# Performance work log

Measured on AMD Instinct MI355X. Metric: run time of the kernel, lower is better.

The kernel has to match this reference:

```python
import jax, jax.numpy as jnp
import numpy as np

B, Q, D_MODEL, H, D_HEAD, PAGE, N_PAGES = 8, 1024, 2048, 16, 128, 256, 8


def setup_inputs() -> dict:
    key = jax.random.key(0)
    ks = jax.random.split(key, 6)
    hidden_states = jax.random.normal(ks[0], (B, Q, D_MODEL), jnp.float32) * 0.02
    W_attn = jax.random.normal(ks[1], (D_MODEL, 3 * D_MODEL), jnp.float32) * 0.02
    b_attn = jnp.zeros((3 * D_MODEL,), jnp.float32)
    W_proj = jax.random.normal(ks[2], (D_MODEL, D_MODEL), jnp.float32) * 0.02
    b_proj = jnp.zeros((D_MODEL,), jnp.float32)
    k_pages = jax.random.normal(ks[3], (N_PAGES, B, H, PAGE, D_HEAD), jnp.float32)
    v_pages = jax.random.normal(ks[4], (N_PAGES, B, H, PAGE, D_HEAD), jnp.float32)
    # every cached page fully valid: (start=0, length=PAGE)
    page_pos = jnp.broadcast_to(jnp.array([0, PAGE], jnp.int32), (N_PAGES, B, 2))
    # current chunk: starts at end of cache, length = q_len
    input_pos = jnp.broadcast_to(jnp.array([N_PAGES * PAGE, Q], jnp.int32), (B, 2))
    return {
        "hidden_states": hidden_states,
        "W_attn": W_attn, "b_attn": b_attn,
        "W_proj": W_proj, "b_proj": b_proj,
        "k_pages": k_pages, "v_pages": v_pages,
        "page_pos": page_pos, "input_pos": input_pos,
    }


def reference(hidden_states, W_attn, b_attn, W_proj, b_proj,
              k_pages, v_pages, page_pos, input_pos):
    dtype = hidden_states.dtype
    NEG = jnp.finfo(dtype).min
    b, q_len, d_model = hidden_states.shape
    n_pages, _, num_heads, page_size, d_head = k_pages.shape
    scale = 1.0 / d_head ** 0.5

    # qkv projection (GPT2 c_attn)
    qkv = hidden_states @ W_attn + b_attn
    q, k_curr, v_curr = jnp.split(qkv, 3, axis=-1)

    def split_heads(x):  # [b, q, d_model] -> [b, h, q, d_head]
        return x.reshape(b, q_len, num_heads, d_head).transpose(0, 2, 1, 3)

    q = split_heads(q)
    k_curr = split_heads(k_curr)
    v_curr = split_heads(v_curr)

    # online softmax state
    m0 = jnp.full((b, num_heads, q_len, 1), NEG, dtype)
    l0 = jnp.zeros((b, num_heads, q_len, 1), dtype)
    acc0 = jnp.zeros((b, num_heads, q_len, d_head), dtype)

    kv_idx = jnp.arange(page_size)

    def page_step(carry, page):
        m, l, acc = carry
        k_p, v_p, pos = page  # [b,h,p,d], [b,h,p,d], [b,2]
        start, length = pos[:, 0], pos[:, 1]
        valid = (kv_idx[None, :] >= start[:, None]) & \
                (kv_idx[None, :] < (start + length)[:, None])  # [b, p]
        s = jnp.einsum('bhqd,bhpd->bhqp', q, k_p) * scale
        s = jnp.where(valid[:, None, None, :], s, NEG)
        m_p = s.max(axis=-1, keepdims=True)
        m_new = jnp.maximum(m, m_p)
        alpha = jnp.exp(m - m_new)
        e = jnp.exp(s - m_new)
        acc = alpha * acc + jnp.einsum('bhqp,bhpd->bhqd', e, v_p)
        l = alpha * l + e.sum(axis=-1, keepdims=True)
        return (m_new, l, acc), None

    (m, l, acc), _ = jax.lax.scan(page_step, (m0, l0, acc0),
                                  (k_pages, v_pages, page_pos))

    # final pass over current chunk: aligned start = 0, length from input_pos
    length = input_pos[:, 1]
    q_idx = jnp.arange(q_len)
    valid = q_idx[None, :] < length[:, None]                     # [b, q]
    causal = jnp.tril(jnp.ones((q_len, q_len), bool))            # keep lower tri
    s = jnp.einsum('bhqd,bhkd->bhqk', q, k_curr) * scale
    keep = valid[:, None, None, :] & causal[None, None, :, :]
    s = jnp.where(keep, s, NEG)
    m_p = s.max(axis=-1, keepdims=True)
    m_new = jnp.maximum(m, m_p)
    alpha = jnp.exp(m - m_new)
    e = jnp.exp(s - m_new)
    acc = alpha * acc + jnp.einsum('bhqk,bhkd->bhqd', e, v_curr)
    l = alpha * l + e.sum(axis=-1, keepdims=True)

    context = acc / jnp.maximum(l, 1e-9)
    context = context.transpose(0, 2, 1, 3).reshape(b, q_len, d_model)
    out = context @ W_proj + b_proj  # resid_dropout is identity in eval
    return out
```

## Files before the change

### kernel.cpp

```cpp
#include <hip/hip_runtime.h>

typedef __bf16 bf16;
typedef __bf16 bf16x8 __attribute__((ext_vector_type(8)));
typedef __bf16 bf16x4 __attribute__((ext_vector_type(4)));
typedef float f32x4 __attribute__((ext_vector_type(4)));
typedef unsigned short u16x4 __attribute__((ext_vector_type(4)));
typedef __attribute__((address_space(3))) const void as3_void;

#define GLOAD16(G,L) __builtin_amdgcn_global_load_lds((__attribute__((address_space(1))) const void*)(G), (__attribute__((address_space(3))) void*)(L), 16, 0, 0)

__global__ void k_cvt_bf16(const float* __restrict__ src, bf16* __restrict__ dst, int n4){
  int i = blockIdx.x*256 + threadIdx.x;
  if (i < n4){
    float4 v = reinterpret_cast<const float4*>(src)[i];
    bf16x4 o; o[0]=(bf16)v.x; o[1]=(bf16)v.y; o[2]=(bf16)v.z; o[3]=(bf16)v.w;
    reinterpret_cast<bf16x4*>(dst)[i] = o;
  }
}

__global__ void k_transpose_cvt(const float* __restrict__ src, bf16* __restrict__ dst, int K, int N){
  __shared__ float tile[32][33];
  int n0 = blockIdx.x*32, k0 = blockIdx.y*32;
  int tx = threadIdx.x & 31, ty = threadIdx.x >> 5;
  #pragma unroll
  for (int i=0;i<32;i+=8)
    tile[ty+i][tx] = src[(size_t)(k0+ty+i)*N + n0+tx];
  __syncthreads();
  #pragma unroll
  for (int i=0;i<32;i+=8)
    dst[(size_t)(n0+ty+i)*K + k0+tx] = (bf16)tile[tx][ty+i];
}

template<int EPI>
__global__ __launch_bounds__(256,2) void k_gemm(
    const bf16* __restrict__ A, const bf16* __restrict__ Bt,
    const float* __restrict__ bias, int N, int K,
    bf16* __restrict__ q_out, bf16* __restrict__ k_out, bf16* __restrict__ v_out,
    float* __restrict__ c_out)
{
  __shared__ bf16 As[2][128*32];
  __shared__ bf16 Bs[2][128*32];
  const int t = threadIdx.x, w = t>>6, l = t&63, g = l>>4;
  const int nb = N>>7;
  const int m0 = (blockIdx.x / nb)<<7, n0 = (blockIdx.x % nb)<<7;
  const bf16* Ab = A  + (size_t)m0*K;
  const bf16* Bb = Bt + (size_t)n0*K;
  size_t sOff[2];
  #pragma unroll
  for (int j=0;j<2;j++){
    int slot = t + (j<<8);
    sOff[j] = (size_t)(slot>>2)*K + ((slot&3)<<3);
  }
  auto stage = [&](int k0, int buf){
    char* ad = (char*)As + (buf<<13) + (w<<10);
    char* bd = (char*)Bs + (buf<<13) + (w<<10);
    #pragma unroll
    for (int j=0;j<2;j++){
      GLOAD16(Ab + sOff[j] + k0, ad + (j<<12));
      GLOAD16(Bb + sOff[j] + k0, bd + (j<<12));
    }
  };
  f32x4 acc[4][4] = {};
  const int mw = (w&1)<<6, nw = (w>>1)<<6;
  const int nk = K>>5;
  int buf = 0;
  stage(0, 0);
  asm volatile("s_waitcnt vmcnt(0)" ::: "memory");
  __syncthreads();
  for (int ks=0; ks<nk; ++ks){
    if (ks+1 < nk) stage((ks+1)<<5, buf^1);
    bf16x8 af[4], bfm[4];
    #pragma unroll
    for (int mf=0;mf<4;mf++)
      af[mf] = *reinterpret_cast<const bf16x8*>(&As[buf][(mw + mf*16 + (l&15))*32 + (g<<3)]);
    #pragma unroll
    for (int nf=0;nf<4;nf++)
      bfm[nf] = *reinterpret_cast<const bf16x8*>(&Bs[buf][(nw + nf*16 + (l&15))*32 + (g<<3)]);
    #pragma unroll
    for (int mf=0;mf<4;mf++)
      #pragma unroll
      for (int nf=0;nf<4;nf++)
        acc[mf][nf] = __builtin_amdgcn_mfma_f32_16x16x32_bf16(af[mf], bfm[nf], acc[mf][nf], 0,0,0);
    asm volatile("s_waitcnt vmcnt(0)" ::: "memory");
    __syncthreads();
    buf ^= 1;
  }
  if constexpr (EPI==0){
    #pragma unroll
    for (int nf=0;nf<4;nf++){
      const int col = n0 + nw + nf*16 + (l&15);
      const int sec = col>>11; const int rem = col&2047;
      const int hh = rem>>7;  const int dd = rem&127;
      bf16* dst = (sec==0) ? q_out : ((sec==1) ? k_out : v_out);
      const float bv = bias[col];
      #pragma unroll
      for (int mf=0;mf<4;mf++)
        #pragma unroll
        for (int ri=0;ri<4;ri++){
          const int row = m0 + mw + mf*16 + (g<<2) + ri;
          const int bb = row>>10, qp = row&1023;
          dst[(((size_t)(bb*16+hh)*1024 + qp)<<7) + dd] = (bf16)(acc[mf][nf][ri] + bv);
        }
    }
  } else {
    #pragma unroll
    for (int nf=0;nf<4;nf++){
      const int col = n0 + nw + nf*16 + (l&15);
      const float bv = bias[col];
      #pragma unroll
      for (int mf=0;mf<4;mf++)
        #pragma unroll
        for (int ri=0;ri<4;ri++){
          const int row = m0 + mw + mf*16 + (g<<2) + ri;
          c_out[(size_t)row*N + col] = acc[mf][nf][ri] + bv;
        }
    }
  }
}

__global__ __launch_bounds__(512) __attribute__((amdgpu_waves_per_eu(4,4))) void k_attn(
    const bf16* __restrict__ qb, const bf16* __restrict__ kb, const bf16* __restrict__ vb,
    const bf16* __restrict__ kpb, const bf16* __restrict__ vpb,
    const int* __restrict__ page_pos, const int* __restrict__ input_pos,
    bf16* __restrict__ ctx)
{
  __shared__ bf16 Ks[2*64*128];
  __shared__ bf16 Vs[2*64*128];
  const int t = threadIdx.x, w = t>>6, l = t&63, g = l>>4, c = l&15;
  const int bid = blockIdx.x;
  const int wg = (bid&7)*128 + (bid>>3);
  const int qt = wg & 7, h = (wg>>3)&15, b = wg>>7;
  const int q0w = (qt<<7) + (w<<4);
  const float scale2 = 0.12751743f;
  const size_t bh = (size_t)(b*16 + h);

  const bf16* qptr = qb + (bh<<17);
  bf16x8 qf[4];
  #pragma unroll
  for (int kc=0;kc<4;kc++)
    qf[kc] = *reinterpret_cast<const bf16x8*>(qptr + ((size_t)(q0w + c)<<7) + kc*32 + (g<<3));

  int kOff[2], vOff[2];
  #pragma unroll
  for (int j=0;j<2;j++){
    const int slot = t + (j<<9);
    {
      const int a = slot<<4; const int r = a>>8; const int co = (a&255) ^ ((r&7)<<4);
      kOff[j] = (r<<7) + (co>>1);
    }
    {
      const int s_ = slot;
      const int p  = ((s_>>6)<<2) | ((s_>>1)&3);
      const int d0 = (((s_>>3)&7)<<4) | ((s_&1)<<3);
      const int pp = (p&32) | ((p&4)<<2) | (((p>>3)&3)<<2) | (p&3);
      vOff[j] = (pp<<7) + d0;
    }
  }
  const bf16* kcb = kb + (bh<<17);
  const bf16* vcb = vb + (bh<<17);
  const int len_b = input_pos[b*2+1];
  const int NT = 32 + ((qt+1)<<1);

  f32x4 o[8] = {};
  float mrow = -1e38f;
  float lsum = 0.f;

  auto tsrc = [&](int T, const bf16*& ks, const bf16*& vs_){
    if (T < 32){
      size_t pb = ((((size_t)(T>>2)<<3) + (size_t)b)*16 + (size_t)h) << 15;
      size_t off = (size_t)(T&3)<<13;
      ks = kpb + pb + off; vs_ = vpb + pb + off;
    } else {
      int kt = T-32; ks = kcb + ((size_t)kt<<13); vs_ = vcb + ((size_t)kt<<13);
    }
  };
  auto stage = [&](int T, int buf){
    const bf16 *ks, *vs_; tsrc(T, ks, vs_);
    char* kd = (char*)Ks + (buf<<14) + (w<<10);
    char* vd = (char*)Vs + (buf<<14) + (w<<10);
    #pragma unroll
    for (int j=0;j<2;j++){
      GLOAD16(ks  + kOff[j], kd + (j<<13));
      GLOAD16(vs_ + vOff[j], vd + (j<<13));
    }
  };

  auto process = [&](int buf, int lo, int hi, bool masked, bool causal, int ktg){
    const char* Kb = (const char*)Ks + (buf<<14);
    const char* Vb = (const char*)Vs + (buf<<14);
    f32x4 s[4] = {};
    #pragma unroll
    for (int kc=0;kc<4;kc++){
      bf16x8 kf[4];
      #pragma unroll
      for (int cb=0;cb<4;cb++){
        const int krow = (cb<<4) + c;
        unsigned a = (unsigned)((krow<<8) + (kc<<6) + (g<<4)); a ^= (unsigned)((krow&7)<<4);
        kf[cb] = *reinterpret_cast<const bf16x8*>(Kb + a);
      }
      __builtin_amdgcn_s_setprio(1);
      #pragma unroll
      for (int cb=0;cb<4;cb++)
        s[cb] = __builtin_amdgcn_mfma_f32_16x16x32_bf16(kf[cb], qf[kc], s[cb], 0,0,0);
      __builtin_amdgcn_s_setprio(0);
    }
    if (masked){
      #pragma unroll
      for (int cb=0;cb<4;cb++)
        #pragma unroll
        for (int ri=0;ri<4;ri++){
          const int kvl = (cb<<4) + (g<<2) + ri;
          bool ok = (kvl >= lo) && (kvl < hi);
          if (causal) ok = ok && ((ktg + kvl) <= (q0w + c));
          s[cb][ri] = ok ? s[cb][ri]*scale2 : -3e38f;
        }
    } else {
      #pragma unroll
      for (int cb=0;cb<4;cb++)
        #pragma unroll
        for (int ri=0;ri<4;ri++)
          s[cb][ri] *= scale2;
    }
    {
      float mx = -3e38f;
      #pragma unroll
      for (int cb=0;cb<4;cb++)
        #pragma unroll
        for (int ri=0;ri<4;ri++) mx = fmaxf(mx, s[cb][ri]);
      mx = fmaxf(mx, __shfl_xor(mx, 16, 64));
      mx = fmaxf(mx, __shfl_xor(mx, 32, 64));
      const int defer = __all(mx - mrow <= 11.5f);
      if (!defer){
        const float mn = fmaxf(mrow, mx);
        const float al = exp2f(mrow - mn);
        mrow = mn;
        lsum *= al;
        #pragma unroll
        for (int ri=0;ri<4;ri++){
          const float av = __shfl(al, (l&48) | ((g<<2)+ri), 64);
          #pragma unroll
          for (int dcb=0;dcb<8;dcb++) o[dcb][ri] *= av;
        }
      }
      float ps = 0.f;
      #pragma unroll
      for (int cb=0;cb<4;cb++)
        #pragma unroll
        for (int ri=0;ri<4;ri++){
          const float e = exp2f(s[cb][ri] - mrow);
          s[cb][ri] = e; ps += e;
        }
      lsum += ps;
    }
    #pragma unroll
    for (int kc=0;kc<2;kc++){
      u16x4 vr0[8], vr1[8];
      #pragma unroll
      for (int dcb=0;dcb<8;dcb++){
        const unsigned sub = ((unsigned)((((kc<<3) + (g<<1))<<3) + dcb)<<7) + ((unsigned)c<<3);
        as3_void* pl = (as3_void*)(Vb + sub);
        asm volatile("ds_read_b64_tr_b16 %0, %2 offset:0\n\t"
                     "ds_read_b64_tr_b16 %1, %2 offset:1024"
                     : "=&v"(vr0[dcb]), "=&v"(vr1[dcb]) : "v"(pl) : "memory");
      }
      bf16x8 pav;
      #pragma unroll
      for (int e=0;e<8;e++)
        pav[e] = (bf16)s[(kc<<1)+(e>>2)][e&3];
      asm volatile("s_waitcnt lgkmcnt(0)" ::: "memory");
      __builtin_amdgcn_sched_barrier(0);
      __builtin_amdgcn_s_setprio(1);
      #pragma unroll
      for (int dcb=0;dcb<8;dcb++){
        union { unsigned short us[8]; bf16x8 v; } uu;
        #pragma unroll
        for (int i=0;i<4;i++){ uu.us[i]=vr0[dcb][i]; uu.us[4+i]=vr1[dcb][i]; }
        o[dcb] = __builtin_amdgcn_mfma_f32_16x16x32_bf16(pav, uu.v, o[dcb], 0,0,0);
      }
      __builtin_amdgcn_s_setprio(0);
    }
  };

  int buf = 0;
  stage(0, 0);
  asm volatile("s_waitcnt vmcnt(0)" ::: "memory");
  __syncthreads();
  for (int T=0; T<NT; ++T){
    if (T+1 < NT) stage(T+1, buf^1);
    int lo=0, hi=64, ktg=0; bool causal=false, masked=false, skip=false;
    if (T < 32){
      const int pg = T>>2, to = T&3;
      const int start = page_pos[(pg*8+b)*2], plen = page_pos[(pg*8+b)*2+1];
      lo = start - (to<<6); hi = start + plen - (to<<6); if (hi>64) hi=64;
      masked = (lo > 0) || (hi < 64);
      skip = (hi <= 0) || (lo >= 64);
    } else {
      const int kt = T-32; ktg = kt<<6;
      hi = len_b - ktg; if (hi>64) hi=64;
      skip = (ktg > q0w + 15) || (hi <= 0);
      causal = (ktg + 63 > q0w);
      masked = causal || (hi < 64);
    }
    if (!skip) process(buf, lo, hi, masked, causal, ktg);
    asm volatile("s_waitcnt vmcnt(0)" ::: "memory");
    __syncthreads();
    buf ^= 1;
  }

  {
    float tl = lsum;
    tl += __shfl_xor(tl, 16, 64);
    tl += __shfl_xor(tl, 32, 64);
    const float inv = 1.f / fmaxf(tl, 1e-9f);
    #pragma unroll
    for (int ri=0;ri<4;ri++){
      const float iv = __shfl(inv, (l&48) | ((g<<2)+ri), 64);
      const int q = q0w + (g<<2) + ri;
      #pragma unroll
      for (int dcb=0;dcb<8;dcb++)
        ctx[(((size_t)(b<<10) + q)<<11) + (h<<7) + (dcb<<4) + c] = (bf16)(o[dcb][ri]*iv);
    }
  }
}

extern "C" void kernel_launch(void* const* d_in, const int* in_sizes, int n_in,
                              void* d_out, int out_size, void* d_ws, size_t ws_size,
                              hipStream_t stream)
{
  const float* hidden  = (const float*)d_in[0];
  const float* W_attn  = (const float*)d_in[1];
  const float* b_attn  = (const float*)d_in[2];
  const float* W_proj  = (const float*)d_in[3];
  const float* b_proj  = (const float*)d_in[4];
  const float* k_pages = (const float*)d_in[5];
  const float* v_pages = (const float*)d_in[6];
  const int*   page_pos  = (const int*)d_in[7];
  const int*   input_pos = (const int*)d_in[8];
  float* out = (float*)d_out;
  char* ws = (char*)d_ws;
  bf16* A1  = (bf16*)(ws);
  bf16* Wt1 = (bf16*)(ws + 33554432);
  bf16* Wt2 = (bf16*)(ws + 58720256);
  bf16* qb  = (bf16*)(ws + 67108864);
  bf16* kb  = (bf16*)(ws + 100663296);
  bf16* vb  = (bf16*)(ws + 134217728);
  bf16* kpb = (bf16*)(ws + 167772160);
  bf16* vpb = (bf16*)(ws + 234881024);
  bf16* ctx = A1;

  k_cvt_bf16<<<16384, 256, 0, stream>>>(hidden, A1, 4194304);
  k_cvt_bf16<<<32768, 256, 0, stream>>>(k_pages, kpb, 8388608);
  k_cvt_bf16<<<32768, 256, 0, stream>>>(v_pages, vpb, 8388608);
  k_transpose_cvt<<<dim3(192,64), 256, 0, stream>>>(W_attn, Wt1, 2048, 6144);
  k_transpose_cvt<<<dim3(64,64),  256, 0, stream>>>(W_proj, Wt2, 2048, 2048);
  k_gemm<0><<<64*48, 256, 0, stream>>>(A1, Wt1, b_attn, 6144, 2048, qb, kb, vb, nullptr);
  k_attn<<<1024, 512, 0, stream>>>(qb, kb, vb, kpb, vpb, page_pos, input_pos, ctx);
  k_gemm<1><<<64*16, 256, 0, stream>>>(ctx, Wt2, b_proj, 2048, 2048, nullptr, nullptr, nullptr, out);
}
```

Before: 768.6 us.

## Rewrite GEMM with 256x256 tiles, 8 waves, swizzled LDS and interleaved staging

Replaces the 128x128, 4-wave GEMM with a 256x256 tile computed by 8 waves, using BK=64 and an XOR-swizzled LDS layout to avoid bank conflicts. The block index is remapped so neighbouring blocks share A and B rows, and each k-step is split into four MFMA clusters. Global-to-LDS prefetch of the next tile is spread between those clusters, with barriers and priority hints around the MFMA runs. This aims to raise arithmetic intensity and overlap loads with compute in both projection GEMMs. The cost is more registers per wave (8x4 accumulators) and fewer blocks (256 for the output projection), which may underfill the GPU.

```diff
diff --git a/kernel.cpp b/kernel.cpp
--- a/kernel.cpp
+++ b/kernel.cpp
@@ -32,87 +32,134 @@
 }
 
 template<int EPI>
-__global__ __launch_bounds__(256,2) void k_gemm(
+__global__ __launch_bounds__(512,2) void k_gemm8(
     const bf16* __restrict__ A, const bf16* __restrict__ Bt,
     const float* __restrict__ bias, int N, int K,
     bf16* __restrict__ q_out, bf16* __restrict__ k_out, bf16* __restrict__ v_out,
     float* __restrict__ c_out)
 {
-  __shared__ bf16 As[2][128*32];
-  __shared__ bf16 Bs[2][128*32];
-  const int t = threadIdx.x, w = t>>6, l = t&63, g = l>>4;
-  const int nb = N>>7;
-  const int m0 = (blockIdx.x / nb)<<7, n0 = (blockIdx.x % nb)<<7;
-  const bf16* Ab = A  + (size_t)m0*K;
-  const bf16* Bb = Bt + (size_t)n0*K;
-  size_t sOff[2];
-  #pragma unroll
-  for (int j=0;j<2;j++){
-    int slot = t + (j<<8);
-    sOff[j] = (size_t)(slot>>2)*K + ((slot&3)<<3);
-  }
-  auto stage = [&](int k0, int buf){
-    char* ad = (char*)As + (buf<<13) + (w<<10);
-    char* bd = (char*)Bs + (buf<<13) + (w<<10);
-    #pragma unroll
-    for (int j=0;j<2;j++){
-      GLOAD16(Ab + sOff[j] + k0, ad + (j<<12));
-      GLOAD16(Bb + sOff[j] + k0, bd + (j<<12));
+  __shared__ bf16 S[2][4][8192];
+  const int t = threadIdx.x, w = t>>6, l = t&63, g = l>>4, c = l&15;
+  const int wm = w>>2, wn = w&3;
+  const int nb = N>>8;
+  const int cpx = gridDim.x>>3;
+  const int swz = (blockIdx.x&7)*cpx + (blockIdx.x>>3);
+  const int m0 = (swz/nb)<<8, n0 = (swz%nb)<<8;
+  const int NK = K>>6;
+  const unsigned xorv = (unsigned)((l&7)<<4);
+
+  const int r0 = t>>3;
+  const int col0 = ((t&7) ^ (r0&7))<<3;
+
+  auto stageA = [&](int kt2){
+    #pragma unroll
+    for (int hh=0; hh<2; ++hh){
+      const bf16* sp = A + (size_t)(m0 + hh*128)*K + (kt2<<6);
+      char* dp = (char*)&S[kt2&1][hh][0];
+      GLOAD16(sp + (size_t)r0*K + col0,      dp + t*16);
+      GLOAD16(sp + (size_t)(r0+64)*K + col0, dp + (t+512)*16);
     }
   };
-  f32x4 acc[4][4] = {};
-  const int mw = (w&1)<<6, nw = (w>>1)<<6;
-  const int nk = K>>5;
-  int buf = 0;
-  stage(0, 0);
+  auto stageB = [&](int kt2){
+    #pragma unroll
+    for (int hh=0; hh<2; ++hh){
+      const bf16* sp = Bt + (size_t)(n0 + hh*128)*K + (kt2<<6);
+      char* dp = (char*)&S[kt2&1][2+hh][0];
+      GLOAD16(sp + (size_t)r0*K + col0,      dp + t*16);
+      GLOAD16(sp + (size_t)(r0+64)*K + col0, dp + (t+512)*16);
+    }
+  };
+
+  f32x4 acc[8][4] = {};
+
+  stageA(0); stageB(0);
   asm volatile("s_waitcnt vmcnt(0)" ::: "memory");
-  __syncthreads();
-  for (int ks=0; ks<nk; ++ks){
-    if (ks+1 < nk) stage((ks+1)<<5, buf^1);
-    bf16x8 af[4], bfm[4];
-    #pragma unroll
-    for (int mf=0;mf<4;mf++)
-      af[mf] = *reinterpret_cast<const bf16x8*>(&As[buf][(mw + mf*16 + (l&15))*32 + (g<<3)]);
-    #pragma unroll
-    for (int nf=0;nf<4;nf++)
-      bfm[nf] = *reinterpret_cast<const bf16x8*>(&Bs[buf][(nw + nf*16 + (l&15))*32 + (g<<3)]);
-    #pragma unroll
-    for (int mf=0;mf<4;mf++)
-      #pragma unroll
-      for (int nf=0;nf<4;nf++)
-        acc[mf][nf] = __builtin_amdgcn_mfma_f32_16x16x32_bf16(af[mf], bfm[nf], acc[mf][nf], 0,0,0);
+  __builtin_amdgcn_s_barrier();
+
+  for (int kt=0; kt<NK; ++kt){
+    const int bufc = kt&1;
+    const char* Ab_ = (const char*)&S[bufc][wm][0];
+    const char* Bb_ = (const char*)&S[bufc][2+(wn>>1)][0];
+    const bool pre = (kt+1 < NK);
+    bf16x8 af[4][2], bfr[2][2];
+
+    auto lda = [&](int mh){
+      #pragma unroll
+      for (int mf=0; mf<4; ++mf)
+        #pragma unroll
+        for (int kk=0; kk<2; ++kk)
+          af[mf][kk] = *reinterpret_cast<const bf16x8*>(Ab_ +
+              (unsigned)((mh*64 + mf*16 + c)*128) + (((unsigned)(kk*64 + g*16)) ^ xorv));
+    };
+    auto ldb = [&](int nh){
+      #pragma unroll
+      for (int nf=0; nf<2; ++nf)
+        #pragma unroll
+        for (int kk=0; kk<2; ++kk)
+          bfr[nf][kk] = *reinterpret_cast<const bf16x8*>(Bb_ +
+              (unsigned)(((wn&1)*64 + nh*32 + nf*16 + c)*128) + (((unsigned)(kk*64 + g*16)) ^ xorv));
+    };
+    auto cluster = [&](int mh, int nh){
+      __builtin_amdgcn_s_barrier();
+      asm volatile("s_waitcnt lgkmcnt(0)" ::: "memory");
+      __builtin_amdgcn_sched_barrier(0);
+      __builtin_amdgcn_s_setprio(1);
+      #pragma unroll
+      for (int mf=0; mf<4; ++mf)
+        #pragma unroll
+        for (int nf=0; nf<2; ++nf)
+          #pragma unroll
+          for (int kk=0; kk<2; ++kk)
+            acc[mh*4+mf][nh*2+nf] =
+              __builtin_amdgcn_mfma_f32_16x16x32_bf16(af[mf][kk], bfr[nf][kk], acc[mh*4+mf][nh*2+nf], 0,0,0);
+      __builtin_amdgcn_s_setprio(0);
+    };
+
+    lda(0); ldb(0);
+    if (pre) stageA(kt+1);
+    cluster(0,0);
+    __builtin_amdgcn_s_barrier();
+    ldb(1);
+    if (pre) stageB(kt+1);
+    cluster(0,1);
+    __builtin_amdgcn_s_barrier();
+    lda(1);
+    cluster(1,1);
+    __builtin_amdgcn_s_barrier();
+    ldb(0);
+    cluster(1,0);
     asm volatile("s_waitcnt vmcnt(0)" ::: "memory");
-    __syncthreads();
-    buf ^= 1;
-  }
+    __builtin_amdgcn_s_barrier();
+  }
+
   if constexpr (EPI==0){
     #pragma unroll
-    for (int nf=0;nf<4;nf++){
-      const int col = n0 + nw + nf*16 + (l&15);
+    for (int NF=0; NF<4; ++NF){
+      const int col = n0 + wn*64 + NF*16 + c;
       const int sec = col>>11; const int rem = col&2047;
-      const int hh = rem>>7;  const int dd = rem&127;
+      const int hhd = rem>>7;  const int dd = rem&127;
       bf16* dst = (sec==0) ? q_out : ((sec==1) ? k_out : v_out);
       const float bv = bias[col];
       #pragma unroll
-      for (int mf=0;mf<4;mf++)
-        #pragma unroll
-        for (int ri=0;ri<4;ri++){
-          const int row = m0 + mw + mf*16 + (g<<2) + ri;
+      for (int MF=0; MF<8; ++MF)
+        #pragma unroll
+        for (int ri=0; ri<4; ++ri){
+          const int row = m0 + wm*128 + MF*16 + (g<<2) + ri;
           const int bb = row>>10, qp = row&1023;
-          dst[(((size_t)(bb*16+hh)*1024 + qp)<<7) + dd] = (bf16)(acc[mf][nf][ri] + bv);
+          dst[(((size_t)(bb*16+hhd)*1024 + qp)<<7) + dd] = (bf16)(acc[MF][NF][ri] + bv);
         }
     }
   } else {
     #pragma unroll
-    for (int nf=0;nf<4;nf++){
-      const int col = n0 + nw + nf*16 + (l&15);
+    for (int NF=0; NF<4; ++NF){
+      const int col = n0 + wn*64 + NF*16 + c;
       const float bv = bias[col];
       #pragma unroll
-      for (int mf=0;mf<4;mf++)
-        #pragma unroll
-        for (int ri=0;ri<4;ri++){
-          const int row = m0 + mw + mf*16 + (g<<2) + ri;
-          c_out[(size_t)row*N + col] = acc[mf][nf][ri] + bv;
+      for (int MF=0; MF<8; ++MF)
+        #pragma unroll
+        for (int ri=0; ri<4; ++ri){
+          const int row = m0 + wm*128 + MF*16 + (g<<2) + ri;
+          c_out[(size_t)row*N + col] = acc[MF][NF][ri] + bv;
         }
     }
   }
@@ -353,7 +400,7 @@
   k_cvt_bf16<<<32768, 256, 0, stream>>>(v_pages, vpb, 8388608);
   k_transpose_cvt<<<dim3(192,64), 256, 0, stream>>>(W_attn, Wt1, 2048, 6144);
   k_transpose_cvt<<<dim3(64,64),  256, 0, stream>>>(W_proj, Wt2, 2048, 2048);
-  k_gemm<0><<<64*48, 256, 0, stream>>>(A1, Wt1, b_attn, 6144, 2048, qb, kb, vb, nullptr);
+  k_gemm8<0><<<768, 512, 0, stream>>>(A1, Wt1, b_attn, 6144, 2048, qb, kb, vb, nullptr);
   k_attn<<<1024, 512, 0, stream>>>(qb, kb, vb, kpb, vpb, page_pos, input_pos, ctx);
-  k_gemm<1><<<64*16, 256, 0, stream>>>(ctx, Wt2, b_proj, 2048, 2048, nullptr, nullptr, nullptr, out);
+  k_gemm8<1><<<256, 512, 0, stream>>>(ctx, Wt2, b_proj, 2048, 2048, nullptr, nullptr, nullptr, out);
 }
```

Measured after the change: 720.2 us. 6.3% less time.
